# Optimization experiments

Hardware: AMD Instinct MI355X
Metric: run time of the kernel (lower is better)

## Reference

```python
import jax, jax.numpy as jnp
import numpy as np

EPS = 1e-5

def _layernorm(x, g, b):
    mu = jnp.mean(x, axis=-1, keepdims=True)
    var = jnp.mean(jnp.square(x - mu), axis=-1, keepdims=True)
    return (x - mu) * jax.lax.rsqrt(var + EPS) * g + b

def setup_inputs() -> dict:
    key = jax.random.key(0)
    ks = jax.random.split(key, 8)
    B, T, D, H = 2, 2048, 1024, 16
    hd = D // H
    s = 0.02
    return {
        "x": jax.random.normal(ks[0], (B, T, D), jnp.float32),
        "wq": jax.random.normal(ks[1], (H, D, hd), jnp.float32) * s,
        "wk": jax.random.normal(ks[2], (H, D, hd), jnp.float32) * s,
        "wv": jax.random.normal(ks[3], (H, D, hd), jnp.float32) * s,
        "w_proj": jax.random.normal(ks[4], (D, D), jnp.float32) * s,
        "b_proj": jnp.zeros((D,), jnp.float32),
        "w_ff1": jax.random.normal(ks[5], (D, 4 * D), jnp.float32) * s,
        "b_ff1": jnp.zeros((4 * D,), jnp.float32),
        "w_ff2": jax.random.normal(ks[6], (4 * D, D), jnp.float32) * s,
        "b_ff2": jnp.zeros((D,), jnp.float32),
        "ln1_g": jnp.ones((D,), jnp.float32),
        "ln1_b": jnp.zeros((D,), jnp.float32),
        "ln2_g": jnp.ones((D,), jnp.float32),
        "ln2_b": jnp.zeros((D,), jnp.float32),
    }

def reference(x, wq, wk, wv, w_proj, b_proj, w_ff1, b_ff1, w_ff2, b_ff2,
              ln1_g, ln1_b, ln2_g, ln2_b):
    B, T, D = x.shape
    H, _, hd = wq.shape
    # --- self-attention sublayer (pre-LN) ---
    h = _layernorm(x, ln1_g, ln1_b)
    # per-head Q/K/V projections batched over heads (math identical to per-head linears)
    q = jnp.einsum('btd,hds->bhts', h, wq)
    k = jnp.einsum('btd,hds->bhts', h, wk)
    v = jnp.einsum('btd,hds->bhts', h, wv)
    att = jnp.einsum('bhts,bhTs->bhtT', q, k) * (hd ** -0.5)  # [B,H,T,T]
    causal = jnp.tril(jnp.ones((T, T), dtype=bool))
    att = jnp.where(causal, att, jnp.float32(-jnp.inf))
    att = jax.nn.softmax(att, axis=-1)
    o = jnp.einsum('bhtT,bhTs->bhts', att, v)                 # [B,H,T,hd]
    o = o.transpose(0, 2, 1, 3).reshape(B, T, H * hd)         # concat heads
    x = x + o @ w_proj + b_proj
    # --- FFN sublayer (pre-LN) ---
    h2 = _layernorm(x, ln2_g, ln2_b)
    ff = jax.nn.relu(h2 @ w_ff1 + b_ff1) @ w_ff2 + b_ff2
    return x + ff
```

## Files before the change

kernel.cpp:

```cpp
#include <hip/hip_runtime.h>

typedef unsigned short u16;
typedef unsigned int   u32;
typedef __bf16 bf16;
typedef bf16 bf16x8 __attribute__((ext_vector_type(8)));
typedef float f32x4 __attribute__((ext_vector_type(4)));
typedef u32 u32x4 __attribute__((ext_vector_type(4)));

__device__ inline u16 f2bf(float f) {
  union { float f; u32 u; } cv; cv.f = f;
  u32 u = cv.u;
  return (u16)((u + 0x7FFFu + ((u >> 16) & 1u)) >> 16);
}

__device__ __forceinline__ void gld16(const void* g, void* l) {
  __builtin_amdgcn_global_load_lds(
      (const __attribute__((address_space(1))) void*)g,
      (__attribute__((address_space(3))) void*)l, 16, 0, 0);
}

__global__ __launch_bounds__(256) void ln_kernel(
    const float* __restrict__ x, const float* __restrict__ g,
    const float* __restrict__ b, u16* __restrict__ out)
{
  const int row = blockIdx.x;
  const int t = threadIdx.x;
  const float4 v = *reinterpret_cast<const float4*>(&x[(size_t)row*1024 + t*4]);
  float s  = v.x + v.y + v.z + v.w;
  float sq = v.x*v.x + v.y*v.y + v.z*v.z + v.w*v.w;
  #pragma unroll
  for (int off = 32; off; off >>= 1) { s += __shfl_down(s, off); sq += __shfl_down(sq, off); }
  __shared__ float red[8];
  const int wave = t >> 6, lane = t & 63;
  if (lane == 0) { red[wave] = s; red[wave + 4] = sq; }
  __syncthreads();
  __shared__ float stats[2];
  if (t == 0) {
    float S  = red[0] + red[1] + red[2] + red[3];
    float SQ = red[4] + red[5] + red[6] + red[7];
    float mu = S * (1.0f/1024.0f);
    float var = SQ * (1.0f/1024.0f) - mu*mu;
    stats[0] = mu; stats[1] = rsqrtf(var + 1e-5f);
  }
  __syncthreads();
  const float mu = stats[0], rv = stats[1];
  const float4 gv = *reinterpret_cast<const float4*>(&g[t*4]);
  const float4 bv = *reinterpret_cast<const float4*>(&b[t*4]);
  u16 o4[4];
  o4[0] = f2bf((v.x - mu)*rv*gv.x + bv.x);
  o4[1] = f2bf((v.y - mu)*rv*gv.y + bv.y);
  o4[2] = f2bf((v.z - mu)*rv*gv.z + bv.z);
  o4[3] = f2bf((v.w - mu)*rv*gv.w + bv.w);
  u32 p0 = (u32)o4[0] | ((u32)o4[1] << 16);
  u32 p1 = (u32)o4[2] | ((u32)o4[3] << 16);
  u32* op = reinterpret_cast<u32*>(&out[(size_t)row*1024 + t*4]);
  op[0] = p0; op[1] = p1;
}

__global__ __launch_bounds__(256) void transpose_cast(
    const float* __restrict__ in, u16* __restrict__ out, int R, int C)
{
  __shared__ float tile[32][33];
  const int tx = threadIdx.x, ty = threadIdx.y;
  const size_t bo = (size_t)blockIdx.z * R * C;
  const int r0 = blockIdx.y * 32, c0 = blockIdx.x * 32;
  #pragma unroll
  for (int j = 0; j < 4; ++j)
    tile[ty + j*8][tx] = in[bo + (size_t)(r0 + ty + j*8)*C + c0 + tx];
  __syncthreads();
  #pragma unroll
  for (int j = 0; j < 4; ++j)
    out[bo + (size_t)(c0 + ty + j*8)*R + r0 + tx] = f2bf(tile[tx][ty + j*8]);
}

__global__ __launch_bounds__(256) void vt_kernel(
    const u16* __restrict__ qkv, u16* __restrict__ vt, int T)
{
  __shared__ u16 tile[32][33];
  const int tx = threadIdx.x, ty = threadIdx.y;
  const int bh = blockIdx.z, b = bh >> 4, h = bh & 15;
  const int r0 = blockIdx.x * 32;
  const int c0 = blockIdx.y * 32;
  const size_t tokbase = (size_t)b * T;
  #pragma unroll
  for (int j = 0; j < 4; ++j)
    tile[ty + j*8][tx] = qkv[(tokbase + r0 + ty + j*8)*3072 + 2048 + h*64 + c0 + tx];
  __syncthreads();
  #pragma unroll
  for (int j = 0; j < 4; ++j)
    vt[((size_t)bh*64 + c0 + ty + j*8)*T + r0 + tx] = tile[tx][ty + j*8];
}

__global__ __launch_bounds__(512, 2) void gemm_128(
    const u16* __restrict__ A, const u16* __restrict__ BT,
    int M, int N, int K,
    const float* __restrict__ bias, const float* __restrict__ resid,
    float* __restrict__ Cout)
{
  __shared__ __align__(16) u16 Alds[2][128*64];
  __shared__ __align__(16) u16 Blds[2][128*64];
  const int t = threadIdx.x;
  const int wave = t >> 6, lane = t & 63;
  const int wm = wave >> 2, wn = wave & 3;
  const int g = lane >> 4, r = lane & 15;
  const int m0 = blockIdx.y * 128, n0 = blockIdx.x * 128;
  const int NTk = K >> 6;

  f32x4 acc[4][2] = {};

  auto STAGE = [&](int buf, int kt) {
    const int k0 = kt << 6;
    #pragma unroll
    for (int p = 0; p < 2; ++p) {
      const int c = t + p*512;
      const int row = c >> 3;
      const int col = (((c & 7) ^ (row & 7)) << 3);
      gld16(&A[(size_t)(m0 + row)*K + k0 + col], &Alds[buf][c*8]);
    }
    #pragma unroll
    for (int p = 0; p < 2; ++p) {
      const int c = t + p*512;
      const int row = c >> 3;
      const int col = (((c & 7) ^ (row & 7)) << 3);
      gld16(&BT[(size_t)(n0 + row)*K + k0 + col], &Blds[buf][c*8]);
    }
  };

  STAGE(0, 0);
  if (NTk > 1) STAGE(1, 1);

  const int csw = (r & 7) << 3;

  for (int kt = 0; kt < NTk; ++kt) {
    const int buf = kt & 1;
    if (kt + 1 < NTk) asm volatile("s_waitcnt vmcnt(4)" ::: "memory");
    else              asm volatile("s_waitcnt vmcnt(0)" ::: "memory");
    __builtin_amdgcn_s_barrier();
    #pragma unroll
    for (int ks = 0; ks < 2; ++ks) {
      bf16x8 af[4], bfr[2];
      #pragma unroll
      for (int i = 0; i < 4; ++i)
        af[i] = *reinterpret_cast<const bf16x8*>(
            &Alds[buf][(wm*64 + i*16 + r)*64 + ((ks*32 + g*8) ^ csw)]);
      #pragma unroll
      for (int j = 0; j < 2; ++j)
        bfr[j] = *reinterpret_cast<const bf16x8*>(
            &Blds[buf][(wn*32 + j*16 + r)*64 + ((ks*32 + g*8) ^ csw)]);
      __builtin_amdgcn_s_setprio(1);
      #pragma unroll
      for (int i = 0; i < 4; ++i)
        #pragma unroll
        for (int j = 0; j < 2; ++j)
          acc[i][j] = __builtin_amdgcn_mfma_f32_16x16x32_bf16(af[i], bfr[j], acc[i][j], 0, 0, 0);
      __builtin_amdgcn_s_setprio(0);
      __builtin_amdgcn_s_barrier();
    }
    if (kt + 2 < NTk) STAGE(buf, kt + 2);
  }

  #pragma unroll
  for (int mi = 0; mi < 4; ++mi) {
    #pragma unroll
    for (int ni = 0; ni < 2; ++ni) {
      #pragma unroll
      for (int i = 0; i < 4; ++i) {
        const int gm = m0 + wm*64 + mi*16 + g*4 + i;
        const int gn = n0 + wn*32 + ni*16 + r;
        const size_t idx = (size_t)gm * N + gn;
        Cout[idx] = acc[mi][ni][i] + bias[gn] + resid[idx];
      }
    }
  }
}

template<int EPI>
__global__ __launch_bounds__(512, 2) void gemm_bt8(
    const u16* __restrict__ A, const u16* __restrict__ BT,
    int M, int N, int K,
    const float* __restrict__ bias, void* __restrict__ Cout)
{
  __shared__ __align__(16) u16 Alds[2][256*64];
  __shared__ __align__(16) u16 Blds[2][256*64];
  const int t = threadIdx.x;
  const int wave = t >> 6, lane = t & 63;
  const int wm = wave >> 2, wn = wave & 3;
  const int g = lane >> 4, r = lane & 15;
  const int m0 = blockIdx.y * 256, n0 = blockIdx.x * 256;
  const int NTk = K >> 6;

  f32x4 acc[8][4] = {};

  auto STAGE = [&](int buf, int kt) {
    const int k0 = kt << 6;
    #pragma unroll
    for (int p = 0; p < 4; ++p) {
      const int c = t + p*512;
      const int row = c >> 3;
      const int col = (((c & 7) ^ (row & 7)) << 3);
      gld16(&A[(size_t)(m0 + row)*K + k0 + col], &Alds[buf][c*8]);
    }
    #pragma unroll
    for (int p = 0; p < 4; ++p) {
      const int c = t + p*512;
      const int row = c >> 3;
      const int col = (((c & 7) ^ (row & 7)) << 3);
      gld16(&BT[(size_t)(n0 + row)*K + k0 + col], &Blds[buf][c*8]);
    }
  };

  STAGE(0, 0);
  if (NTk > 1) STAGE(1, 1);

  const int csw = (r & 7) << 3;

  for (int kt = 0; kt < NTk; ++kt) {
    const int buf = kt & 1;
    if (kt + 1 < NTk) asm volatile("s_waitcnt vmcnt(8)" ::: "memory");
    else              asm volatile("s_waitcnt vmcnt(0)" ::: "memory");
    __builtin_amdgcn_s_barrier();
    #pragma unroll
    for (int p = 0; p < 4; ++p) {
      const int ks = p >> 1, mih = p & 1;
      bf16x8 af[4], bfr[4];
      #pragma unroll
      for (int i = 0; i < 4; ++i) {
        af[i] = *reinterpret_cast<const bf16x8*>(
            &Alds[buf][(wm*128 + (mih*4 + i)*16 + r)*64 + ((ks*32 + g*8) ^ csw)]);
        bfr[i] = *reinterpret_cast<const bf16x8*>(
            &Blds[buf][(wn*64 + i*16 + r)*64 + ((ks*32 + g*8) ^ csw)]);
      }
      __builtin_amdgcn_s_setprio(1);
      #pragma unroll
      for (int i = 0; i < 4; ++i)
        #pragma unroll
        for (int j = 0; j < 4; ++j)
          acc[mih*4 + i][j] =
              __builtin_amdgcn_mfma_f32_16x16x32_bf16(af[i], bfr[j], acc[mih*4 + i][j], 0, 0, 0);
      __builtin_amdgcn_s_setprio(0);
      __builtin_amdgcn_s_barrier();
    }
    if (kt + 2 < NTk) STAGE(buf, kt + 2);
  }

  #pragma unroll
  for (int mi = 0; mi < 8; ++mi) {
    #pragma unroll
    for (int ni = 0; ni < 4; ++ni) {
      #pragma unroll
      for (int i = 0; i < 4; ++i) {
        const int gm = m0 + wm*128 + mi*16 + g*4 + i;
        const int gn = n0 + wn*64 + ni*16 + r;
        const size_t idx = (size_t)gm * N + gn;
        float v = acc[mi][ni][i];
        if (EPI == 0) {
          const float sc = (gn < 1024) ? 0.18033688011112042f : 1.0f;
          ((u16*)Cout)[idx] = f2bf(v * sc);
        } else {
          v += bias[gn];
          ((u16*)Cout)[idx] = f2bf(v > 0.f ? v : 0.f);
        }
      }
    }
  }
}

__global__ __launch_bounds__(256, 4) void attn_kernel(
    const u16* __restrict__ qkv, const u16* __restrict__ vt,
    u16* __restrict__ o, int T)
{
  const int bid = blockIdx.x;
  const int swz = (bid & 7) * 128 + (bid >> 3);
  const int idx = swz & 31;
  const int qa  = (idx & 1) ? ((idx - 1) >> 1) : (31 - (idx >> 1));
  const int bh  = swz >> 5;
  const int b = bh >> 4, h = bh & 15;
  const int t = threadIdx.x;
  const int wave = t >> 6, lane = t & 63;
  const int g = lane >> 4, r = lane & 15;
  const size_t tokbase = (size_t)b * T;
  const int q0 = qa*64 + wave*16;

  __shared__ __align__(16) u16 Klds[2][64*64];
  __shared__ __align__(16) u16 Vlds[2][64*64];
  __shared__ __align__(16) u16 P[4][16*64];

  bf16x8 qf[2];
  #pragma unroll
  for (int ks = 0; ks < 2; ++ks)
    qf[ks] = *reinterpret_cast<const bf16x8*>(
        &qkv[(tokbase + q0 + r)*3072 + h*64 + ks*32 + g*8]);

  bf16x8 ones;
  #pragma unroll
  for (int i = 0; i < 8; ++i) ones[i] = (bf16)1.0f;

  f32x4 acc_o[4] = {};
  f32x4 acc_l = {};

  const int nkv = qa + 1;

  auto STAGE = [&](int buf, int kb) {
    const int kv0 = kb*64;
    #pragma unroll
    for (int p = 0; p < 2; ++p) {
      const int c2 = t + p*256;
      const int row = c2 >> 3;
      const int scol = ((c2 & 7) ^ (row & 7)) << 3;
      gld16(&qkv[(tokbase + kv0 + row)*3072 + 1024 + h*64 + scol], &Klds[buf][c2*8]);
      gld16(&vt[((size_t)bh*64 + row)*T + kv0 + scol], &Vlds[buf][c2*8]);
    }
  };

  STAGE(0, 0);
  int cur = 0;
  for (int kb = 0; kb < nkv; ++kb) {
    __syncthreads();
    if (kb + 1 < nkv) STAGE(cur ^ 1, kb + 1);
    const int kv0 = kb*64;
    const bool diag = (kb == qa);
    const int cb = (r & 7) << 3;

    f32x4 s[4] = {};
    #pragma unroll
    for (int nb = 0; nb < 4; ++nb) {
      #pragma unroll
      for (int ks = 0; ks < 2; ++ks) {
        bf16x8 kf = *reinterpret_cast<const bf16x8*>(
            &Klds[cur][(nb*16 + r)*64 + ((ks*32 + g*8) ^ cb)]);
        s[nb] = __builtin_amdgcn_mfma_f32_16x16x32_bf16(qf[ks], kf, s[nb], 0, 0, 0);
      }
    }
    #pragma unroll
    for (int i = 0; i < 4; ++i) {
      const int prow = g*4 + i;
      const int pcb = (prow & 7) << 3;
      #pragma unroll
      for (int nb = 0; nb < 4; ++nb) {
        float pv = __builtin_amdgcn_exp2f(s[nb][i]);
        if (diag && (kv0 + nb*16 + r > q0 + prow)) pv = 0.f;
        P[wave][prow*64 + ((nb*16 + r) ^ pcb)] = f2bf(pv);
      }
    }
    #pragma unroll
    for (int ks = 0; ks < 2; ++ks) {
      bf16x8 pf = *reinterpret_cast<const bf16x8*>(
          &P[wave][r*64 + ((ks*32 + g*8) ^ cb)]);
      acc_l = __builtin_amdgcn_mfma_f32_16x16x32_bf16(pf, ones, acc_l, 0, 0, 0);
      #pragma unroll
      for (int nt = 0; nt < 4; ++nt) {
        bf16x8 vf = *reinterpret_cast<const bf16x8*>(
            &Vlds[cur][(nt*16 + r)*64 + ((ks*32 + g*8) ^ cb)]);
        acc_o[nt] = __builtin_amdgcn_mfma_f32_16x16x32_bf16(pf, vf, acc_o[nt], 0, 0, 0);
      }
    }
    cur ^= 1;
  }
  #pragma unroll
  for (int i = 0; i < 4; ++i) {
    const float inv = 1.0f / acc_l[i];
    const size_t rowo = (tokbase + q0 + g*4 + i) * 1024;
    #pragma unroll
    for (int nt = 0; nt < 4; ++nt)
      o[rowo + h*64 + nt*16 + r] = f2bf(acc_o[nt][i] * inv);
  }
}

extern "C" void kernel_launch(void* const* d_in, const int* in_sizes, int n_in,
                              void* d_out, int out_size, void* d_ws, size_t ws_size,
                              hipStream_t stream)
{
  const float* x      = (const float*)d_in[0];
  const float* wq     = (const float*)d_in[1];
  const float* wk     = (const float*)d_in[2];
  const float* wv     = (const float*)d_in[3];
  const float* w_proj = (const float*)d_in[4];
  const float* b_proj = (const float*)d_in[5];
  const float* w_ff1  = (const float*)d_in[6];
  const float* b_ff1  = (const float*)d_in[7];
  const float* w_ff2  = (const float*)d_in[8];
  const float* b_ff2  = (const float*)d_in[9];
  const float* ln1_g  = (const float*)d_in[10];
  const float* ln1_b  = (const float*)d_in[11];
  const float* ln2_g  = (const float*)d_in[12];
  const float* ln2_b  = (const float*)d_in[13];

  const int T = 2048;
  const int NT = 4096;

  char* ws = (char*)d_ws;
  u16* Wbuf   = (u16*)(ws);
  u16* hbuf   = (u16*)(ws + ((size_t)8  << 20));
  u16* qkvbuf = (u16*)(ws + ((size_t)16 << 20));
  u16* obuf   = (u16*)(ws + ((size_t)40 << 20));
  u16* ff1buf = qkvbuf;
  u16* vtbuf  = Wbuf;
  float* x1   = (float*)d_out;

  ln_kernel<<<dim3(NT), dim3(256), 0, stream>>>(x, ln1_g, ln1_b, hbuf);
  transpose_cast<<<dim3(2, 32, 16), dim3(32, 8), 0, stream>>>(wq, Wbuf + 0*1024*1024, 1024, 64);
  transpose_cast<<<dim3(2, 32, 16), dim3(32, 8), 0, stream>>>(wk, Wbuf + 1*1024*1024, 1024, 64);
  transpose_cast<<<dim3(2, 32, 16), dim3(32, 8), 0, stream>>>(wv, Wbuf + 2*1024*1024, 1024, 64);
  gemm_bt8<0><<<dim3(12, 16), dim3(512), 0, stream>>>(hbuf, Wbuf, NT, 3072, 1024, nullptr, qkvbuf);
  vt_kernel<<<dim3(64, 2, 32), dim3(32, 8), 0, stream>>>(qkvbuf, vtbuf, T);
  attn_kernel<<<dim3(1024), dim3(256), 0, stream>>>(qkvbuf, vtbuf, obuf, T);
  transpose_cast<<<dim3(32, 32, 1), dim3(32, 8), 0, stream>>>(w_proj, Wbuf, 1024, 1024);
  gemm_128<<<dim3(8, 32), dim3(512), 0, stream>>>(obuf, Wbuf, NT, 1024, 1024, b_proj, x, x1);
  ln_kernel<<<dim3(NT), dim3(256), 0, stream>>>(x1, ln2_g, ln2_b, hbuf);
  transpose_cast<<<dim3(128, 32, 1), dim3(32, 8), 0, stream>>>(w_ff1, Wbuf, 1024, 4096);
  gemm_bt8<2><<<dim3(16, 16), dim3(512), 0, stream>>>(hbuf, Wbuf, NT, 4096, 1024, b_ff1, ff1buf);
  transpose_cast<<<dim3(32, 128, 1), dim3(32, 8), 0, stream>>>(w_ff2, Wbuf, 4096, 1024);
  gemm_128<<<dim3(8, 32), dim3(512), 0, stream>>>(ff1buf, Wbuf, NT, 1024, 4096, b_ff2, x1, (float*)d_out);
}
```

Baseline: 267.9 us.

## Split-K FF2 GEMM with atomic accumulation, fold bias+residual into LN2

Result: faster. 262.2 us (-2.1%).

```diff
diff --git a/kernel.cpp b/kernel.cpp
--- a/kernel.cpp
+++ b/kernel.cpp
@@ -19,9 +19,11 @@
       (__attribute__((address_space(3))) void*)l, 16, 0, 0);
 }
 
+template<bool ADDB>
 __global__ __launch_bounds__(256) void ln_kernel(
     const float* __restrict__ x, const float* __restrict__ g,
-    const float* __restrict__ b, u16* __restrict__ out)
+    const float* __restrict__ b, u16* __restrict__ out,
+    const float* __restrict__ badd, float* __restrict__ xwb)
 {
   const int row = blockIdx.x;
   const int t = threadIdx.x;
@@ -55,6 +57,12 @@
   u32 p1 = (u32)o4[2] | ((u32)o4[3] << 16);
   u32* op = reinterpret_cast<u32*>(&out[(size_t)row*1024 + t*4]);
   op[0] = p0; op[1] = p1;
+  if (ADDB) {
+    const float4 av = *reinterpret_cast<const float4*>(&badd[t*4]);
+    float4 w;
+    w.x = v.x + av.x; w.y = v.y + av.y; w.z = v.z + av.z; w.w = v.w + av.w;
+    *reinterpret_cast<float4*>(&xwb[(size_t)row*1024 + t*4]) = w;
+  }
 }
 
 __global__ __launch_bounds__(256) void transpose_cast(
@@ -169,6 +177,90 @@
         const int gn = n0 + wn*32 + ni*16 + r;
         const size_t idx = (size_t)gm * N + gn;
         Cout[idx] = acc[mi][ni][i] + bias[gn] + resid[idx];
+      }
+    }
+  }
+}
+
+__global__ __launch_bounds__(512, 2) void gemm_128_sk(
+    const u16* __restrict__ A, const u16* __restrict__ BT,
+    int M, int N, int K, float* __restrict__ Cout)
+{
+  __shared__ __align__(16) u16 Alds[2][128*64];
+  __shared__ __align__(16) u16 Blds[2][128*64];
+  const int bid = blockIdx.x;
+  const int s = bid >> 3;
+  const int n0 = (s & 7) * 128;
+  const int m0 = (((s >> 3) & 3) * 8 + (bid & 7)) * 128;
+  const int kbase = (s >> 5) * (K >> 1);
+  const int t = threadIdx.x;
+  const int wave = t >> 6, lane = t & 63;
+  const int wm = wave >> 2, wn = wave & 3;
+  const int g = lane >> 4, r = lane & 15;
+  const int NTk = K >> 7;
+
+  f32x4 acc[4][2] = {};
+
+  auto STAGE = [&](int buf, int kt) {
+    const int k0 = kbase + (kt << 6);
+    #pragma unroll
+    for (int p = 0; p < 2; ++p) {
+      const int c = t + p*512;
+      const int row = c >> 3;
+      const int col = (((c & 7) ^ (row & 7)) << 3);
+      gld16(&A[(size_t)(m0 + row)*K + k0 + col], &Alds[buf][c*8]);
+    }
+    #pragma unroll
+    for (int p = 0; p < 2; ++p) {
+      const int c = t + p*512;
+      const int row = c >> 3;
+      const int col = (((c & 7) ^ (row & 7)) << 3);
+      gld16(&BT[(size_t)(n0 + row)*K + k0 + col], &Blds[buf][c*8]);
+    }
+  };
+
+  STAGE(0, 0);
+  if (NTk > 1) STAGE(1, 1);
+
+  const int csw = (r & 7) << 3;
+
+  for (int kt = 0; kt < NTk; ++kt) {
+    const int buf = kt & 1;
+    if (kt + 1 < NTk) asm volatile("s_waitcnt vmcnt(4)" ::: "memory");
+    else              asm volatile("s_waitcnt vmcnt(0)" ::: "memory");
+    __builtin_amdgcn_s_barrier();
+    #pragma unroll
+    for (int ks = 0; ks < 2; ++ks) {
+      bf16x8 af[4], bfr[2];
+      #pragma unroll
+      for (int i = 0; i < 4; ++i)
+        af[i] = *reinterpret_cast<const bf16x8*>(
+            &Alds[buf][(wm*64 + i*16 + r)*64 + ((ks*32 + g*8) ^ csw)]);
+      #pragma unroll
+      for (int j = 0; j < 2; ++j)
+        bfr[j] = *reinterpret_cast<const bf16x8*>(
+            &Blds[buf][(wn*32 + j*16 + r)*64 + ((ks*32 + g*8) ^ csw)]);
+      __builtin_amdgcn_s_setprio(1);
+      #pragma unroll
+      for (int i = 0; i < 4; ++i)
+        #pragma unroll
+        for (int j = 0; j < 2; ++j)
+          acc[i][j] = __builtin_amdgcn_mfma_f32_16x16x32_bf16(af[i], bfr[j], acc[i][j], 0, 0, 0);
+      __builtin_amdgcn_s_setprio(0);
+      __builtin_amdgcn_s_barrier();
+    }
+    if (kt + 2 < NTk) STAGE(buf, kt + 2);
+  }
+
+  #pragma unroll
+  for (int mi = 0; mi < 4; ++mi) {
+    #pragma unroll
+    for (int ni = 0; ni < 2; ++ni) {
+      #pragma unroll
+      for (int i = 0; i < 4; ++i) {
+        const int gm = m0 + wm*64 + mi*16 + g*4 + i;
+        const int gn = n0 + wn*32 + ni*16 + r;
+        unsafeAtomicAdd(&Cout[(size_t)gm * N + gn], acc[mi][ni][i]);
       }
     }
   }
@@ -397,7 +489,7 @@
   u16* vtbuf  = Wbuf;
   float* x1   = (float*)d_out;
 
-  ln_kernel<<<dim3(NT), dim3(256), 0, stream>>>(x, ln1_g, ln1_b, hbuf);
+  ln_kernel<false><<<dim3(NT), dim3(256), 0, stream>>>(x, ln1_g, ln1_b, hbuf, nullptr, nullptr);
   transpose_cast<<<dim3(2, 32, 16), dim3(32, 8), 0, stream>>>(wq, Wbuf + 0*1024*1024, 1024, 64);
   transpose_cast<<<dim3(2, 32, 16), dim3(32, 8), 0, stream>>>(wk, Wbuf + 1*1024*1024, 1024, 64);
   transpose_cast<<<dim3(2, 32, 16), dim3(32, 8), 0, stream>>>(wv, Wbuf + 2*1024*1024, 1024, 64);
@@ -406,9 +498,9 @@
   attn_kernel<<<dim3(1024), dim3(256), 0, stream>>>(qkvbuf, vtbuf, obuf, T);
   transpose_cast<<<dim3(32, 32, 1), dim3(32, 8), 0, stream>>>(w_proj, Wbuf, 1024, 1024);
   gemm_128<<<dim3(8, 32), dim3(512), 0, stream>>>(obuf, Wbuf, NT, 1024, 1024, b_proj, x, x1);
-  ln_kernel<<<dim3(NT), dim3(256), 0, stream>>>(x1, ln2_g, ln2_b, hbuf);
+  ln_kernel<true><<<dim3(NT), dim3(256), 0, stream>>>(x1, ln2_g, ln2_b, hbuf, b_ff2, x1);
   transpose_cast<<<dim3(128, 32, 1), dim3(32, 8), 0, stream>>>(w_ff1, Wbuf, 1024, 4096);
   gemm_bt8<2><<<dim3(16, 16), dim3(512), 0, stream>>>(hbuf, Wbuf, NT, 4096, 1024, b_ff1, ff1buf);
   transpose_cast<<<dim3(32, 128, 1), dim3(32, 8), 0, stream>>>(w_ff2, Wbuf, 4096, 1024);
-  gemm_128<<<dim3(8, 32), dim3(512), 0, stream>>>(ff1buf, Wbuf, NT, 1024, 4096, b_ff2, x1, (float*)d_out);
-}
+  gemm_128_sk<<<dim3(512), dim3(512), 0, stream>>>(ff1buf, Wbuf, NT, 1024, 4096, (float*)d_out);
+}
```
